# Kernel optimization log

Hardware: AMD Instinct MI355X
Metric: run time of the kernel (lower is better)

The kernel has to match this reference:

```python
import jax, jax.numpy as jnp
import numpy as np

B, S, H, F, E, TOPK = 2, 2048, 1024, 2048, 8, 2


def setup_inputs() -> dict:
    key = jax.random.key(0)
    k1, k2, k3, k4, k5 = jax.random.split(key, 5)
    scale_h = 1.0 / np.sqrt(H)
    scale_f = 1.0 / np.sqrt(F)
    return {
        "hidden_states": jax.random.normal(k1, (B, S, H), dtype=jnp.float32),
        "gate_w": jax.random.normal(k2, (E, H), dtype=jnp.float32) * scale_h,
        "w1": jax.random.normal(k3, (E, F, H), dtype=jnp.float32) * scale_h,
        "w2": jax.random.normal(k4, (E, H, F), dtype=jnp.float32) * scale_f,
        "w3": jax.random.normal(k5, (E, F, H), dtype=jnp.float32) * scale_h,
    }


def reference(hidden_states, gate_w, w1, w2, w3):
    b, s, h = hidden_states.shape
    x = hidden_states.reshape(-1, h)                      # [T, H]
    T = x.shape[0]
    router_logits = x @ gate_w.T                          # [T, E]
    probs = jax.nn.softmax(router_logits.astype(jnp.float32), axis=-1)
    rw, sel = jax.lax.top_k(probs, TOPK)                  # [T, k]
    rw = rw / jnp.sum(rw, axis=-1, keepdims=True)
    rw = rw.astype(x.dtype)
    # combine weights [T, E]: routing weight where selected, else 0
    combine = jnp.zeros((T, E), dtype=x.dtype).at[
        jnp.arange(T)[:, None], sel].add(rw)
    # dense dispatch: compute every expert on all tokens, mask via combine
    h1 = jnp.einsum('th,efh->etf', x, w1)                 # [E, T, F]
    h3 = jnp.einsum('th,efh->etf', x, w3)
    gated = jax.nn.silu(h1) * h3
    out_e = jnp.einsum('etf,ehf->eth', gated, w2)         # [E, T, H]
    final = jnp.einsum('eth,te->th', out_e, combine)      # [T, H]
    return final.reshape(b, s, h), router_logits
```

## Files before the change

kernel.cpp:

```cpp
#include <hip/hip_runtime.h>
#include <hip/hip_bf16.h>

#define TT 4096
#define HH 1024
#define FF 2048
#define EE 8
#define NC32 2048
#define LDSU 32768

typedef short short8_t __attribute__((ext_vector_type(8)));
typedef float f32x4 __attribute__((ext_vector_type(4)));

__device__ __forceinline__ unsigned short f2b(float f) {
  union { float f; unsigned u; } v; v.f = f;
  return (unsigned short)((v.u + 0x7fffu + ((v.u >> 16) & 1u)) >> 16);
}

__device__ __forceinline__ void gload16(const unsigned short* g, void* l) {
  __builtin_amdgcn_global_load_lds(
      (const __attribute__((address_space(1))) void*)g,
      (__attribute__((address_space(3))) void*)l, 16, 0, 0);
}

#define FENCE asm volatile("" ::: "memory")

__device__ __forceinline__ void conv_ilp(const float* __restrict__ src,
                                         unsigned short* __restrict__ dst,
                                         int c, int tid) {
  size_t base = (size_t)c * 8192 + tid * 4;
  float4 v[8];
#pragma unroll
  for (int j = 0; j < 8; ++j)
    v[j] = *reinterpret_cast<const float4*>(src + base + j * 1024);
#pragma unroll
  for (int j = 0; j < 8; ++j) {
    ushort4 b4;
    b4.x = f2b(v[j].x); b4.y = f2b(v[j].y); b4.z = f2b(v[j].z); b4.w = f2b(v[j].w);
    *reinterpret_cast<ushort4*>(dst + base + j * 1024) = b4;
  }
}

__global__ __launch_bounds__(256) void front_kernel(
    const float* __restrict__ x, const float* __restrict__ gw,
    const float* __restrict__ w1, const float* __restrict__ w3,
    const float* __restrict__ w2,
    float* __restrict__ out_logits, float* __restrict__ final_out,
    unsigned short* __restrict__ xbf,
    unsigned short* __restrict__ w1bf, unsigned short* __restrict__ w3bf,
    unsigned short* __restrict__ w2bf,
    int* __restrict__ sel01, float2* __restrict__ w01)
{
  int tid = threadIdx.x;
  int b = blockIdx.x;
  if (b >= TT) {
    int cb = b - TT;
    if (cb < NC32)          conv_ilp(w1, w1bf, cb, tid);
    else if (cb < 2 * NC32) conv_ilp(w3, w3bf, cb - NC32, tid);
    else                    conv_ilp(w2, w2bf, cb - 2 * NC32, tid);
    return;
  }
  int t = b;

  __shared__ float xs[HH];
  __shared__ float lg[EE];

  float4 v = reinterpret_cast<const float4*>(x + (size_t)t * HH)[tid];
  xs[tid * 4 + 0] = v.x; xs[tid * 4 + 1] = v.y;
  xs[tid * 4 + 2] = v.z; xs[tid * 4 + 3] = v.w;
  ushort4 b4;
  b4.x = f2b(v.x); b4.y = f2b(v.y); b4.z = f2b(v.z); b4.w = f2b(v.w);
  reinterpret_cast<ushort4*>(xbf + (size_t)t * HH)[tid] = b4;
  float4 z4; z4.x = z4.y = z4.z = z4.w = 0.f;
  reinterpret_cast<float4*>(final_out + (size_t)t * HH)[tid] = z4;
  __syncthreads();

  int lane = tid & 63, wv = tid >> 6;
  for (int e = wv; e < EE; e += 4) {
    float s = 0.f;
    const float* g = gw + (size_t)e * HH;
#pragma unroll
    for (int j = 0; j < HH / 64; ++j) s += xs[lane + j * 64] * g[lane + j * 64];
#pragma unroll
    for (int off = 32; off > 0; off >>= 1) s += __shfl_down(s, off);
    if (lane == 0) lg[e] = s;
  }
  __syncthreads();

  if (tid < 8) out_logits[(size_t)t * EE + tid] = lg[tid];
  if (tid == 0) {
    float l[EE];
#pragma unroll
    for (int e = 0; e < EE; ++e) l[e] = lg[e];
    int e0 = 0;
#pragma unroll
    for (int e = 1; e < EE; ++e) if (l[e] > l[e0]) e0 = e;
    int e1 = -1;
#pragma unroll
    for (int e = 0; e < EE; ++e) if (e != e0 && (e1 < 0 || l[e] > l[e1])) e1 = e;
    float p1 = expf(l[e1] - l[e0]);
    float w0 = 1.f / (1.f + p1);
    float w1v = p1 * w0;
    sel01[t] = e0 | (e1 << 8);
    w01[t] = make_float2(w0, w1v);
  }
}

__global__ __launch_bounds__(256) void build_kernel(
    const int* __restrict__ sel01, const float2* __restrict__ w01,
    int* __restrict__ counts, int* __restrict__ tokidx, float* __restrict__ rww)
{
  int e = blockIdx.x;
  int tid = threadIdx.x, lane = tid & 63, wv = tid >> 6;
  __shared__ int wsum[4];
  int base = 0;
  for (int t0 = 0; t0 < TT; t0 += 256) {
    int t = t0 + tid;
    int s = sel01[t];
    int e0 = s & 255, e1 = (s >> 8) & 255;
    bool hit = (e0 == e) || (e1 == e);
    float w = 0.f;
    if (hit) { float2 ww = w01[t]; w = (e0 == e) ? ww.x : ww.y; }
    unsigned long long m = __ballot(hit);
    int wpre = __popcll(m & ((1ull << lane) - 1));
    if (lane == 63) wsum[wv] = wpre + (hit ? 1 : 0);
    __syncthreads();
    int wbase = base;
    for (int q = 0; q < wv; ++q) wbase += wsum[q];
    if (hit) {
      int pos = wbase + wpre;
      tokidx[e * TT + pos] = t;
      rww[e * TT + pos] = w;
    }
    base += wsum[0] + wsum[1] + wsum[2] + wsum[3];
    __syncthreads();
  }
  if (tid == 0) counts[e] = base;
}

__global__ __launch_bounds__(256) void conv_kernel(
    const float* __restrict__ src, unsigned short* __restrict__ dst)
{
  conv_ilp(src, dst, blockIdx.x, threadIdx.x);
}

__global__ __launch_bounds__(256) void up_gate_kernel(
    const unsigned short* __restrict__ xbf,
    const unsigned short* __restrict__ w1bf, const unsigned short* __restrict__ w3bf,
    const int* __restrict__ counts, const int* __restrict__ tokidx,
    unsigned short* __restrict__ gated)
{
  int e = blockIdx.z;
  int n = counts[e];
  int row0 = blockIdx.y * 128;
  if (row0 >= n) return;
  int fbase = blockIdx.x * 64;

  int pe = 0;
  for (int q = 0; q < e; ++q) pe += (counts[q] + 127) & ~127;

  __shared__ __align__(16) char lds[2 * LDSU];

  int tid = threadIdx.x;
  int lane = tid & 63, wv = tid >> 6;
  int sb = (tid & 7) ^ ((tid >> 3) & 7);

  const unsigned short* ga[4];
#pragma unroll
  for (int j = 0; j < 4; ++j) {
    int r = min(row0 + (tid >> 3) + 32 * j, n - 1);
    ga[j] = xbf + (size_t)tokidx[e * TT + r] * HH + sb * 8;
  }
  const unsigned short* gb1[2];
  const unsigned short* gb3[2];
#pragma unroll
  for (int j = 0; j < 2; ++j) {
    size_t rw_ = (size_t)e * FF + fbase + (tid >> 3) + 32 * j;
    gb1[j] = w1bf + rw_ * HH + sb * 8;
    gb3[j] = w3bf + rw_ * HH + sb * 8;
  }

  int wr = (wv >> 1) * 64, wc = (wv & 1) * 32;
  int fr = lane & 15, kq = lane >> 4, l7 = lane & 7;

  f32x4 acc1[4][2], acc3[4][2];
#pragma unroll
  for (int m = 0; m < 4; ++m)
#pragma unroll
    for (int nn = 0; nn < 2; ++nn) { acc1[m][nn] = (f32x4)0.f; acc3[m][nn] = (f32x4)0.f; }

#define UG_STAGE(T, SOFF) do {                                                     \
    _Pragma("unroll") for (int j = 0; j < 4; ++j)                                  \
      gload16(ga[j] + (T) * 64, lds + (SOFF) + j * 4096 + wv * 1024);              \
    _Pragma("unroll") for (int j = 0; j < 2; ++j) {                                \
      gload16(gb1[j] + (T) * 64, lds + (SOFF) + 16384 + j * 4096 + wv * 1024);     \
      gload16(gb3[j] + (T) * 64, lds + (SOFF) + 24576 + j * 4096 + wv * 1024);     \
    } } while (0)

#define UG_PHASE(SOFF, KS) do {                                                             \
    int bswz = (((KS) * 4 + kq) ^ l7) * 16;                                                 \
    short8_t a[4], b1f[2], b3f[2];                                                          \
    _Pragma("unroll") for (int m = 0; m < 4; ++m)                                           \
      a[m] = *(const short8_t*)(lds + (SOFF) + (wr + m * 16 + fr) * 128 + bswz);            \
    _Pragma("unroll") for (int nn = 0; nn < 2; ++nn) {                                      \
      b1f[nn] = *(const short8_t*)(lds + (SOFF) + 16384 + (wc + nn * 16 + fr) * 128 + bswz); \
      b3f[nn] = *(const short8_t*)(lds + (SOFF) + 24576 + (wc + nn * 16 + fr) * 128 + bswz); \
    }                                                                                       \
    __builtin_amdgcn_s_setprio(1);                                                          \
    _Pragma("unroll") for (int m = 0; m < 4; ++m)                                           \
      _Pragma("unroll") for (int nn = 0; nn < 2; ++nn) {                                    \
        acc1[m][nn] = __builtin_amdgcn_mfma_f32_16x16x32_bf16(a[m], b1f[nn], acc1[m][nn], 0, 0, 0); \
        acc3[m][nn] = __builtin_amdgcn_mfma_f32_16x16x32_bf16(a[m], b3f[nn], acc3[m][nn], 0, 0, 0); \
      }                                                                                     \
    __builtin_amdgcn_s_setprio(0);                                                          \
  } while (0)

#define UG_NT 16
#define UG_ITER(T, SOFF) do {                                          \
    if ((T) < UG_NT - 1) asm volatile("s_waitcnt vmcnt(8)" ::: "memory"); \
    else                 asm volatile("s_waitcnt vmcnt(0)" ::: "memory"); \
    __builtin_amdgcn_s_barrier(); FENCE;                               \
    UG_PHASE(SOFF, 0);                                                 \
    FENCE; __builtin_amdgcn_s_barrier(); FENCE;                        \
    UG_PHASE(SOFF, 1);                                                 \
    FENCE; __builtin_amdgcn_s_barrier(); FENCE;                        \
    if ((T) + 2 < UG_NT) UG_STAGE((T) + 2, SOFF);                      \
  } while (0)

  UG_STAGE(0, 0);
  UG_STAGE(1, LDSU);
  for (int t2 = 0; t2 < UG_NT; t2 += 2) { UG_ITER(t2, 0); UG_ITER(t2 + 1, LDSU); }
#undef UG_STAGE
#undef UG_PHASE
#undef UG_ITER

  size_t gbase = ((size_t)pe + row0) * FF + fbase;
#pragma unroll
  for (int m = 0; m < 4; ++m) {
#pragma unroll
    for (int nn = 0; nn < 2; ++nn) {
      f32x4 h1v = acc1[m][nn], h3v = acc3[m][nn];
#pragma unroll
      for (int j = 0; j < 4; ++j) {
        float z = h1v[j];
        float val = (z / (1.f + expf(-z))) * h3v[j];
        int r = wr + m * 16 + (lane >> 4) * 4 + j;
        int c = wc + nn * 16 + fr;
        gated[gbase + (size_t)r * FF + c] = f2b(val);
      }
    }
  }
}

__global__ __launch_bounds__(256) void down_kernel(
    const unsigned short* __restrict__ gated,
    const unsigned short* __restrict__ w2bf,
    const int* __restrict__ counts, const int* __restrict__ tokidx,
    const float* __restrict__ rww,
    float* __restrict__ final_out)
{
  int e = blockIdx.z;
  int n = counts[e];
  int row0 = blockIdx.y * 128;
  if (row0 >= n) return;
  int hbase = blockIdx.x * 128;
  int valid = min(128, n - row0);

  int pe = 0;
  for (int q = 0; q < e; ++q) pe += (counts[q] + 127) & ~127;

  __shared__ __align__(16) char lds[2 * LDSU];

  int tid = threadIdx.x;
  int lane = tid & 63, wv = tid >> 6;
  int sb = (tid & 7) ^ ((tid >> 3) & 7);

  const unsigned short* ga[4];
  const unsigned short* gb[4];
#pragma unroll
  for (int j = 0; j < 4; ++j) {
    ga[j] = gated + ((size_t)pe + row0 + (tid >> 3) + 32 * j) * FF + sb * 8;
    gb[j] = w2bf + ((size_t)e * HH + hbase + (tid >> 3) + 32 * j) * FF + sb * 8;
  }

  int wr = (wv >> 1) * 64, wc = (wv & 1) * 64;
  int fr = lane & 15, kq = lane >> 4, l7 = lane & 7;

  f32x4 acc[4][4];
#pragma unroll
  for (int m = 0; m < 4; ++m)
#pragma unroll
    for (int nn = 0; nn < 4; ++nn) acc[m][nn] = (f32x4)0.f;

#define DN_STAGE(T, SOFF) do {                                                   \
    _Pragma("unroll") for (int j = 0; j < 4; ++j) {                              \
      gload16(ga[j] + (T) * 64, lds + (SOFF) + j * 4096 + wv * 1024);            \
      gload16(gb[j] + (T) * 64, lds + (SOFF) + 16384 + j * 4096 + wv * 1024);    \
    } } while (0)

#define DN_PHASE(SOFF, KS) do {                                                            \
    int bswz = (((KS) * 4 + kq) ^ l7) * 16;                                                \
    short8_t a[4], bf[4];                                                                  \
    _Pragma("unroll") for (int m = 0; m < 4; ++m)                                          \
      a[m] = *(const short8_t*)(lds + (SOFF) + (wr + m * 16 + fr) * 128 + bswz);           \
    _Pragma("unroll") for (int nn = 0; nn < 4; ++nn)                                       \
      bf[nn] = *(const short8_t*)(lds + (SOFF) + 16384 + (wc + nn * 16 + fr) * 128 + bswz); \
    __builtin_amdgcn_s_setprio(1);                                                         \
    _Pragma("unroll") for (int m = 0; m < 4; ++m)                                          \
      _Pragma("unroll") for (int nn = 0; nn < 4; ++nn)                                     \
        acc[m][nn] = __builtin_amdgcn_mfma_f32_16x16x32_bf16(a[m], bf[nn], acc[m][nn], 0, 0, 0); \
    __builtin_amdgcn_s_setprio(0);                                                         \
  } while (0)

#define DN_NT 32
#define DN_ITER(T, SOFF) do {                                          \
    if ((T) < DN_NT - 1) asm volatile("s_waitcnt vmcnt(8)" ::: "memory"); \
    else                 asm volatile("s_waitcnt vmcnt(0)" ::: "memory"); \
    __builtin_amdgcn_s_barrier(); FENCE;                               \
    DN_PHASE(SOFF, 0);                                                 \
    FENCE; __builtin_amdgcn_s_barrier(); FENCE;                        \
    DN_PHASE(SOFF, 1);                                                 \
    FENCE; __builtin_amdgcn_s_barrier(); FENCE;                        \
    if ((T) + 2 < DN_NT) DN_STAGE((T) + 2, SOFF);                      \
  } while (0)

  DN_STAGE(0, 0);
  DN_STAGE(1, LDSU);
  for (int t2 = 0; t2 < DN_NT; t2 += 2) { DN_ITER(t2, 0); DN_ITER(t2 + 1, LDSU); }
#undef DN_STAGE
#undef DN_PHASE
#undef DN_ITER

#pragma unroll
  for (int m = 0; m < 4; ++m) {
    int rbase = wr + m * 16 + (lane >> 4) * 4;
#pragma unroll
    for (int j = 0; j < 4; ++j) {
      int r = rbase + j;
      if (r < valid) {
        int t = tokidx[e * TT + row0 + r];
        float w = rww[e * TT + row0 + r];
#pragma unroll
        for (int nn = 0; nn < 4; ++nn) {
          int c = hbase + wc + nn * 16 + fr;
          atomicAdd(&final_out[(size_t)t * HH + c], w * acc[m][nn][j]);
        }
      }
    }
  }
}

extern "C" void kernel_launch(void* const* d_in, const int* in_sizes, int n_in,
                              void* d_out, int out_size, void* d_ws, size_t ws_size,
                              hipStream_t stream) {
  const float* x  = (const float*)d_in[0];
  const float* gw = (const float*)d_in[1];
  const float* w1 = (const float*)d_in[2];
  const float* w2 = (const float*)d_in[3];
  const float* w3 = (const float*)d_in[4];

  float* final_out  = (float*)d_out;
  float* out_logits = final_out + (size_t)TT * HH;

  char* ws = (char*)d_ws;
  int*    counts = (int*)(ws + 0);
  int*    sel01  = (int*)(ws + 1024);
  float2* w01    = (float2*)(ws + 20480);
  int*    tokidx = (int*)(ws + 53248);
  float*  rww    = (float*)(ws + 184320);
  unsigned short* xbf   = (unsigned short*)(ws + 315392);
  unsigned short* w1bf  = (unsigned short*)(ws + 8704000);
  unsigned short* w3bf  = (unsigned short*)(ws + 42258432);
  unsigned short* gated = (unsigned short*)(ws + 75812864);
  const size_t base_end = 113561600;
  bool big = ws_size >= base_end + 33554432;
  unsigned short* w2bf = big ? (unsigned short*)(ws + base_end) : w1bf;

  int nconvblk = (big ? 3 : 2) * NC32;
  front_kernel<<<TT + nconvblk, 256, 0, stream>>>(
      x, gw, w1, w3, w2, out_logits, final_out, xbf, w1bf, w3bf, w2bf,
      sel01, w01);
  build_kernel<<<EE, 256, 0, stream>>>(sel01, w01, counts, tokidx, rww);
  up_gate_kernel<<<dim3(FF / 64, TT / 128, EE), 256, 0, stream>>>(
      xbf, w1bf, w3bf, counts, tokidx, gated);
  if (!big) conv_kernel<<<NC32, 256, 0, stream>>>(w2, w1bf);
  down_kernel<<<dim3(HH / 128, TT / 128, EE), 256, 0, stream>>>(
      gated, w2bf, counts, tokidx, rww, final_out);
}
```

Baseline: 253.8 us.

## Load A operand directly from global into registers, bypass LDS staging

Both expert GEMM kernels now stream only the weight (B) tiles through the double-buffered LDS. Each lane reads its A-operand fragments (token activations or gated rows) straight from global memory into registers at the start of each k-step. This halves LDS usage, which may raise occupancy, and drops one barrier per iteration. In exchange, the A loads are not prefetched ahead of use, so their global latency sits directly in front of the MFMAs. Each row is also read in 64-byte pieces rather than through coalesced full-row copies.

New measurement: 387.4 us. +52.6%, slower.

```diff
diff --git a/kernel.cpp b/kernel.cpp
--- a/kernel.cpp
+++ b/kernel.cpp
@@ -6,7 +6,6 @@
 #define FF 2048
 #define EE 8
 #define NC32 2048
-#define LDSU 32768
 
 typedef short short8_t __attribute__((ext_vector_type(8)));
 typedef float f32x4 __attribute__((ext_vector_type(4)));
@@ -158,18 +157,12 @@
   int pe = 0;
   for (int q = 0; q < e; ++q) pe += (counts[q] + 127) & ~127;
 
-  __shared__ __align__(16) char lds[2 * LDSU];
+  __shared__ __align__(16) char lds[2 * 16384];
 
   int tid = threadIdx.x;
   int lane = tid & 63, wv = tid >> 6;
   int sb = (tid & 7) ^ ((tid >> 3) & 7);
 
-  const unsigned short* ga[4];
-#pragma unroll
-  for (int j = 0; j < 4; ++j) {
-    int r = min(row0 + (tid >> 3) + 32 * j, n - 1);
-    ga[j] = xbf + (size_t)tokidx[e * TT + r] * HH + sb * 8;
-  }
   const unsigned short* gb1[2];
   const unsigned short* gb3[2];
 #pragma unroll
@@ -182,53 +175,59 @@
   int wr = (wv >> 1) * 64, wc = (wv & 1) * 32;
   int fr = lane & 15, kq = lane >> 4, l7 = lane & 7;
 
+  const unsigned short* pA[4];
+#pragma unroll
+  for (int m = 0; m < 4; ++m) {
+    int r = min(row0 + wr + m * 16 + fr, n - 1);
+    pA[m] = xbf + (size_t)tokidx[e * TT + r] * HH + kq * 8;
+  }
+
   f32x4 acc1[4][2], acc3[4][2];
 #pragma unroll
   for (int m = 0; m < 4; ++m)
 #pragma unroll
     for (int nn = 0; nn < 2; ++nn) { acc1[m][nn] = (f32x4)0.f; acc3[m][nn] = (f32x4)0.f; }
 
-#define UG_STAGE(T, SOFF) do {                                                     \
-    _Pragma("unroll") for (int j = 0; j < 4; ++j)                                  \
-      gload16(ga[j] + (T) * 64, lds + (SOFF) + j * 4096 + wv * 1024);              \
-    _Pragma("unroll") for (int j = 0; j < 2; ++j) {                                \
-      gload16(gb1[j] + (T) * 64, lds + (SOFF) + 16384 + j * 4096 + wv * 1024);     \
-      gload16(gb3[j] + (T) * 64, lds + (SOFF) + 24576 + j * 4096 + wv * 1024);     \
+#define UG_STAGE(T, SOFF) do {                                                   \
+    _Pragma("unroll") for (int j = 0; j < 2; ++j) {                              \
+      gload16(gb1[j] + (T) * 64, lds + (SOFF) + j * 4096 + wv * 1024);           \
+      gload16(gb3[j] + (T) * 64, lds + (SOFF) + 8192 + j * 4096 + wv * 1024);    \
     } } while (0)
 
-#define UG_PHASE(SOFF, KS) do {                                                             \
+#define UG_PHASE(SOFF, KS, AV) do {                                                         \
     int bswz = (((KS) * 4 + kq) ^ l7) * 16;                                                 \
-    short8_t a[4], b1f[2], b3f[2];                                                          \
-    _Pragma("unroll") for (int m = 0; m < 4; ++m)                                           \
-      a[m] = *(const short8_t*)(lds + (SOFF) + (wr + m * 16 + fr) * 128 + bswz);            \
+    short8_t b1f[2], b3f[2];                                                                \
     _Pragma("unroll") for (int nn = 0; nn < 2; ++nn) {                                      \
-      b1f[nn] = *(const short8_t*)(lds + (SOFF) + 16384 + (wc + nn * 16 + fr) * 128 + bswz); \
-      b3f[nn] = *(const short8_t*)(lds + (SOFF) + 24576 + (wc + nn * 16 + fr) * 128 + bswz); \
+      b1f[nn] = *(const short8_t*)(lds + (SOFF) + (wc + nn * 16 + fr) * 128 + bswz);        \
+      b3f[nn] = *(const short8_t*)(lds + (SOFF) + 8192 + (wc + nn * 16 + fr) * 128 + bswz); \
     }                                                                                       \
     __builtin_amdgcn_s_setprio(1);                                                          \
     _Pragma("unroll") for (int m = 0; m < 4; ++m)                                           \
       _Pragma("unroll") for (int nn = 0; nn < 2; ++nn) {                                    \
-        acc1[m][nn] = __builtin_amdgcn_mfma_f32_16x16x32_bf16(a[m], b1f[nn], acc1[m][nn], 0, 0, 0); \
-        acc3[m][nn] = __builtin_amdgcn_mfma_f32_16x16x32_bf16(a[m], b3f[nn], acc3[m][nn], 0, 0, 0); \
+        acc1[m][nn] = __builtin_amdgcn_mfma_f32_16x16x32_bf16(AV[m], b1f[nn], acc1[m][nn], 0, 0, 0); \
+        acc3[m][nn] = __builtin_amdgcn_mfma_f32_16x16x32_bf16(AV[m], b3f[nn], acc3[m][nn], 0, 0, 0); \
       }                                                                                     \
     __builtin_amdgcn_s_setprio(0);                                                          \
   } while (0)
 
 #define UG_NT 16
 #define UG_ITER(T, SOFF) do {                                          \
-    if ((T) < UG_NT - 1) asm volatile("s_waitcnt vmcnt(8)" ::: "memory"); \
-    else                 asm volatile("s_waitcnt vmcnt(0)" ::: "memory"); \
+    asm volatile("s_waitcnt vmcnt(4)" ::: "memory");                   \
     __builtin_amdgcn_s_barrier(); FENCE;                               \
-    UG_PHASE(SOFF, 0);                                                 \
-    FENCE; __builtin_amdgcn_s_barrier(); FENCE;                        \
-    UG_PHASE(SOFF, 1);                                                 \
+    short8_t av0_[4], av1_[4];                                         \
+    _Pragma("unroll") for (int m = 0; m < 4; ++m) {                    \
+      av0_[m] = *(const short8_t*)(pA[m] + (T) * 64);                  \
+      av1_[m] = *(const short8_t*)(pA[m] + (T) * 64 + 32);             \
+    }                                                                  \
+    UG_PHASE(SOFF, 0, av0_);                                           \
+    UG_PHASE(SOFF, 1, av1_);                                           \
     FENCE; __builtin_amdgcn_s_barrier(); FENCE;                        \
     if ((T) + 2 < UG_NT) UG_STAGE((T) + 2, SOFF);                      \
   } while (0)
 
   UG_STAGE(0, 0);
-  UG_STAGE(1, LDSU);
-  for (int t2 = 0; t2 < UG_NT; t2 += 2) { UG_ITER(t2, 0); UG_ITER(t2 + 1, LDSU); }
+  UG_STAGE(1, 16384);
+  for (int t2 = 0; t2 < UG_NT; t2 += 2) { UG_ITER(t2, 0); UG_ITER(t2 + 1, 16384); }
 #undef UG_STAGE
 #undef UG_PHASE
 #undef UG_ITER
@@ -268,23 +267,25 @@
   int pe = 0;
   for (int q = 0; q < e; ++q) pe += (counts[q] + 127) & ~127;
 
-  __shared__ __align__(16) char lds[2 * LDSU];
+  __shared__ __align__(16) char lds[2 * 16384];
 
   int tid = threadIdx.x;
   int lane = tid & 63, wv = tid >> 6;
   int sb = (tid & 7) ^ ((tid >> 3) & 7);
 
-  const unsigned short* ga[4];
   const unsigned short* gb[4];
 #pragma unroll
-  for (int j = 0; j < 4; ++j) {
-    ga[j] = gated + ((size_t)pe + row0 + (tid >> 3) + 32 * j) * FF + sb * 8;
+  for (int j = 0; j < 4; ++j)
     gb[j] = w2bf + ((size_t)e * HH + hbase + (tid >> 3) + 32 * j) * FF + sb * 8;
-  }
 
   int wr = (wv >> 1) * 64, wc = (wv & 1) * 64;
   int fr = lane & 15, kq = lane >> 4, l7 = lane & 7;
 
+  const unsigned short* pA[4];
+#pragma unroll
+  for (int m = 0; m < 4; ++m)
+    pA[m] = gated + ((size_t)pe + row0 + wr + m * 16 + fr) * FF + kq * 8;
+
   f32x4 acc[4][4];
 #pragma unroll
   for (int m = 0; m < 4; ++m)
@@ -292,40 +293,40 @@
     for (int nn = 0; nn < 4; ++nn) acc[m][nn] = (f32x4)0.f;
 
 #define DN_STAGE(T, SOFF) do {                                                   \
-    _Pragma("unroll") for (int j = 0; j < 4; ++j) {                              \
-      gload16(ga[j] + (T) * 64, lds + (SOFF) + j * 4096 + wv * 1024);            \
-      gload16(gb[j] + (T) * 64, lds + (SOFF) + 16384 + j * 4096 + wv * 1024);    \
-    } } while (0)
-
-#define DN_PHASE(SOFF, KS) do {                                                            \
+    _Pragma("unroll") for (int j = 0; j < 4; ++j)                                \
+      gload16(gb[j] + (T) * 64, lds + (SOFF) + j * 4096 + wv * 1024);            \
+  } while (0)
+
+#define DN_PHASE(SOFF, KS, AV) do {                                                        \
     int bswz = (((KS) * 4 + kq) ^ l7) * 16;                                                \
-    short8_t a[4], bf[4];                                                                  \
-    _Pragma("unroll") for (int m = 0; m < 4; ++m)                                          \
-      a[m] = *(const short8_t*)(lds + (SOFF) + (wr + m * 16 + fr) * 128 + bswz);           \
+    short8_t bf[4];                                                                        \
     _Pragma("unroll") for (int nn = 0; nn < 4; ++nn)                                       \
-      bf[nn] = *(const short8_t*)(lds + (SOFF) + 16384 + (wc + nn * 16 + fr) * 128 + bswz); \
+      bf[nn] = *(const short8_t*)(lds + (SOFF) + (wc + nn * 16 + fr) * 128 + bswz);        \
     __builtin_amdgcn_s_setprio(1);                                                         \
     _Pragma("unroll") for (int m = 0; m < 4; ++m)                                          \
       _Pragma("unroll") for (int nn = 0; nn < 4; ++nn)                                     \
-        acc[m][nn] = __builtin_amdgcn_mfma_f32_16x16x32_bf16(a[m], bf[nn], acc[m][nn], 0, 0, 0); \
+        acc[m][nn] = __builtin_amdgcn_mfma_f32_16x16x32_bf16(AV[m], bf[nn], acc[m][nn], 0, 0, 0); \
     __builtin_amdgcn_s_setprio(0);                                                         \
   } while (0)
 
 #define DN_NT 32
 #define DN_ITER(T, SOFF) do {                                          \
-    if ((T) < DN_NT - 1) asm volatile("s_waitcnt vmcnt(8)" ::: "memory"); \
-    else                 asm volatile("s_waitcnt vmcnt(0)" ::: "memory"); \
+    asm volatile("s_waitcnt vmcnt(4)" ::: "memory");                   \
     __builtin_amdgcn_s_barrier(); FENCE;                               \
-    DN_PHASE(SOFF, 0);                                                 \
-    FENCE; __builtin_amdgcn_s_barrier(); FENCE;                        \
-    DN_PHASE(SOFF, 1);                                                 \
+    short8_t av0_[4], av1_[4];                                         \
+    _Pragma("unroll") for (int m = 0; m < 4; ++m) {                    \
+      av0_[m] = *(const short8_t*)(pA[m] + (T) * 64);                  \
+      av1_[m] = *(const short8_t*)(pA[m] + (T) * 64 + 32);             \
+    }                                                                  \
+    DN_PHASE(SOFF, 0, av0_);                                           \
+    DN_PHASE(SOFF, 1, av1_);                                           \
     FENCE; __builtin_amdgcn_s_barrier(); FENCE;                        \
     if ((T) + 2 < DN_NT) DN_STAGE((T) + 2, SOFF);                      \
   } while (0)
 
   DN_STAGE(0, 0);
-  DN_STAGE(1, LDSU);
-  for (int t2 = 0; t2 < DN_NT; t2 += 2) { DN_ITER(t2, 0); DN_ITER(t2 + 1, LDSU); }
+  DN_STAGE(1, 16384);
+  for (int t2 = 0; t2 < DN_NT; t2 += 2) { DN_ITER(t2, 0); DN_ITER(t2 + 1, 16384); }
 #undef DN_STAGE
 #undef DN_PHASE
 #undef DN_ITER
```

## Replace atomic scatter-add in down projection with per-slot stores and combine kernel

Applied to the files above, without the earlier changes.

The down-projection kernel now writes each token's weighted expert output into one of two slot buffers, picked by whether the expert is the token's first or second choice, instead of atomically adding into the zeroed output. A new elementwise kernel sums the two slots into the final output, and the zero-initialisation in the front kernel is dropped. This removes float atomic contention and read-modify-write traffic. In exchange it adds an extra pass over two 16 MB buffers and reuses the w3 bf16 workspace as slot storage after up_gate has finished with it.

Result: no change. 251.9 us (-0.8%).

```diff
diff --git a/kernel.cpp b/kernel.cpp
--- a/kernel.cpp
+++ b/kernel.cpp
@@ -44,7 +44,7 @@
     const float* __restrict__ x, const float* __restrict__ gw,
     const float* __restrict__ w1, const float* __restrict__ w3,
     const float* __restrict__ w2,
-    float* __restrict__ out_logits, float* __restrict__ final_out,
+    float* __restrict__ out_logits,
     unsigned short* __restrict__ xbf,
     unsigned short* __restrict__ w1bf, unsigned short* __restrict__ w3bf,
     unsigned short* __restrict__ w2bf,
@@ -70,8 +70,6 @@
   ushort4 b4;
   b4.x = f2b(v.x); b4.y = f2b(v.y); b4.z = f2b(v.z); b4.w = f2b(v.w);
   reinterpret_cast<ushort4*>(xbf + (size_t)t * HH)[tid] = b4;
-  float4 z4; z4.x = z4.y = z4.z = z4.w = 0.f;
-  reinterpret_cast<float4*>(final_out + (size_t)t * HH)[tid] = z4;
   __syncthreads();
 
   int lane = tid & 63, wv = tid >> 6;
@@ -143,6 +141,17 @@
   conv_ilp(src, dst, blockIdx.x, threadIdx.x);
 }
 
+__global__ __launch_bounds__(256) void combine_kernel(
+    const float4* __restrict__ s0, const float4* __restrict__ s1,
+    float4* __restrict__ out)
+{
+  size_t i = (size_t)blockIdx.x * 256 + threadIdx.x;
+  float4 a = s0[i], b = s1[i];
+  float4 r;
+  r.x = a.x + b.x; r.y = a.y + b.y; r.z = a.z + b.z; r.w = a.w + b.w;
+  out[i] = r;
+}
+
 __global__ __launch_bounds__(256) void up_gate_kernel(
     const unsigned short* __restrict__ xbf,
     const unsigned short* __restrict__ w1bf, const unsigned short* __restrict__ w3bf,
@@ -255,8 +264,8 @@
     const unsigned short* __restrict__ gated,
     const unsigned short* __restrict__ w2bf,
     const int* __restrict__ counts, const int* __restrict__ tokidx,
-    const float* __restrict__ rww,
-    float* __restrict__ final_out)
+    const float* __restrict__ rww, const int* __restrict__ sel01,
+    float* __restrict__ slots)
 {
   int e = blockIdx.z;
   int n = counts[e];
@@ -339,10 +348,12 @@
       if (r < valid) {
         int t = tokidx[e * TT + row0 + r];
         float w = rww[e * TT + row0 + r];
+        int sl = ((sel01[t] & 255) == e) ? 0 : 1;
+        float* dst = slots + (size_t)sl * TT * HH + (size_t)t * HH;
 #pragma unroll
         for (int nn = 0; nn < 4; ++nn) {
           int c = hbase + wc + nn * 16 + fr;
-          atomicAdd(&final_out[(size_t)t * HH + c], w * acc[m][nn][j]);
+          dst[c] = w * acc[m][nn][j];
         }
       }
     }
@@ -374,15 +385,18 @@
   const size_t base_end = 113561600;
   bool big = ws_size >= base_end + 33554432;
   unsigned short* w2bf = big ? (unsigned short*)(ws + base_end) : w1bf;
+  float* slots = (float*)w3bf;
 
   int nconvblk = (big ? 3 : 2) * NC32;
   front_kernel<<<TT + nconvblk, 256, 0, stream>>>(
-      x, gw, w1, w3, w2, out_logits, final_out, xbf, w1bf, w3bf, w2bf,
-      sel01, w01);
+      x, gw, w1, w3, w2, out_logits, xbf, w1bf, w3bf, w2bf, sel01, w01);
   build_kernel<<<EE, 256, 0, stream>>>(sel01, w01, counts, tokidx, rww);
   up_gate_kernel<<<dim3(FF / 64, TT / 128, EE), 256, 0, stream>>>(
       xbf, w1bf, w3bf, counts, tokidx, gated);
   if (!big) conv_kernel<<<NC32, 256, 0, stream>>>(w2, w1bf);
   down_kernel<<<dim3(HH / 128, TT / 128, EE), 256, 0, stream>>>(
-      gated, w2bf, counts, tokidx, rww, final_out);
-}
+      gated, w2bf, counts, tokidx, rww, sel01, slots);
+  combine_kernel<<<TT * HH / 1024, 256, 0, stream>>>(
+      (const float4*)slots, (const float4*)(slots + (size_t)TT * HH),
+      (float4*)final_out);
+}
```
